# Performance work log

Hardware: AMD Instinct MI355X
Metric: run time of the kernel (lower is better)

The kernel has to match this reference:

```python
import jax, jax.numpy as jnp
import numpy as np

HEADS = 16
KV_HEADS = 8
DIMS = 64
IN_DIMS = 1024
B, S = 2, 2048


def rope(x):
    # RoPE applied over the FULL flattened last dim (heads*dims), as in the source.
    seq_len, dim = x.shape[-2], x.shape[-1]
    thetas = 1.0 / 10000 ** (jnp.arange(0, dim, 2) / dim)          # [dim/2]
    ang = jnp.arange(1, seq_len + 1)[:, None] * thetas[None, :]    # [S, dim/2] (positions start at 1)
    cos, sin = jnp.cos(ang), jnp.sin(ang)
    xe, xo = x[..., ::2], x[..., 1::2]
    real = xe * cos - xo * sin
    imag = xe * sin + xo * cos
    return jnp.stack([real, imag], axis=-1).reshape(x.shape)


def setup_inputs() -> dict:
    key = jax.random.key(0)
    k1, k2, k3, k4, k5 = jax.random.split(key, 5)
    q = jax.random.normal(k1, (B, S, IN_DIMS), dtype=jnp.float32)
    sd = 1.0 / np.sqrt(IN_DIMS)
    Wq = jax.random.normal(k2, (IN_DIMS, HEADS * DIMS), dtype=jnp.float32) * sd
    Wk = jax.random.normal(k3, (IN_DIMS, KV_HEADS * DIMS), dtype=jnp.float32) * sd
    Wv = jax.random.normal(k4, (IN_DIMS, KV_HEADS * DIMS), dtype=jnp.float32) * sd
    Wo = jax.random.normal(k5, (HEADS * DIMS, IN_DIMS), dtype=jnp.float32) / np.sqrt(HEADS * DIMS)
    return {"q": q, "Wq": Wq, "Wk": Wk, "Wv": Wv, "Wo": Wo}


def reference(q, Wq, Wk, Wv, Wo):
    batch, seq_len, in_dims = q.shape
    kv = q  # self-attention (kv=None path)
    xq = rope(q @ Wq)            # [B, S, H*D], RoPE over flattened dim
    xk = rope(kv @ Wk)           # [B, S, Hk*D]
    xv = kv @ Wv                 # [B, S, Hk*D]
    # element-wise repeat(2) on last axis, exactly as source (interleaved duplication)
    xk = jnp.repeat(xk, 2, axis=-1)   # [B, S, H*D]
    xv = jnp.repeat(xv, 2, axis=-1)
    xq = xq.reshape(batch, seq_len, HEADS, DIMS).transpose(0, 2, 1, 3)  # [B,H,S,D]
    xk = xk.reshape(batch, seq_len, HEADS, DIMS).transpose(0, 2, 3, 1)  # [B,H,D,S]
    xv = xv.reshape(batch, seq_len, HEADS, DIMS).transpose(0, 2, 1, 3)  # [B,H,S,D]
    scale = (DIMS / HEADS) ** (-0.5)  # source uses dims/heads, not 1/sqrt(dims)
    scores = jax.nn.softmax((xq @ xk) * scale, axis=-1)  # [B,H,S,S]
    out = (scores @ xv).transpose(0, 2, 1, 3).reshape(batch, seq_len, -1)
    return out @ Wo
```

## Files before the change

### kernel.cpp

```cpp
#include <hip/hip_runtime.h>
#include <hip/hip_bf16.h>
#include <math.h>

#define HEADS 16
#define KV_HEADS 8
#define DIMS 64
#define IN_DIMS 1024
#define BATCH 2
#define SEQ 2048

typedef __attribute__((ext_vector_type(8))) short short8;
typedef __attribute__((ext_vector_type(4))) float f32x4;
typedef __attribute__((ext_vector_type(4))) unsigned int u32x4;
typedef __attribute__((ext_vector_type(2))) unsigned int u32x2;

__device__ __forceinline__ short f2bf(float f) {
    __hip_bfloat16 h = __float2bfloat16(f);
    return *reinterpret_cast<short*>(&h);
}

__device__ __forceinline__ unsigned int cvtpk(float a, float b) {
    unsigned int r;
    asm("v_cvt_pk_bf16_f32 %0, %1, %2" : "=v"(r) : "v"(a), "v"(b));
    return r;
}

__device__ __forceinline__ void gl_lds16(const void* g, void* l) {
    __builtin_amdgcn_global_load_lds(
        (const __attribute__((address_space(1))) unsigned int*)g,
        (__attribute__((address_space(3))) unsigned int*)l, 16, 0, 0);
}

#define LOG2_10000 13.287712379549449f
#define CSCALE (0.5f * 1.4426950408889634f)

__global__ __launch_bounds__(256) void prep_weights(
    const float* __restrict__ Wq, const float* __restrict__ Wk,
    const float* __restrict__ Wv, const float* __restrict__ Wo,
    short* __restrict__ WT, short* __restrict__ WoPt,
    const float* __restrict__ qin, short* __restrict__ Abf)
{
    __shared__ float t[32][33];
    int z = blockIdx.z;
    if (z >= 4) {
        int i = (z - 4) * 1024 + blockIdx.y * 32 + blockIdx.x;
        size_t idx = ((size_t)i * 256 + threadIdx.x) * 8;
        float4 a = *(const float4*)(qin + idx);
        float4 c = *(const float4*)(qin + idx + 4);
        u32x4 s = { cvtpk(a.x, a.y), cvtpk(a.z, a.w),
                    cvtpk(c.x, c.y), cvtpk(c.z, c.w) };
        *(u32x4*)(Abf + idx) = s;
        return;
    }
    int bx = blockIdx.x * 32, by = blockIdx.y * 32;
    int x = threadIdx.x & 31, y = threadIdx.x >> 5;
    if (z == 3) {
        if (by >= 512) return;
        #pragma unroll
        for (int i = 0; i < 32; i += 8) {
            int d = by + y + i;
            t[y + i][x] = Wo[(size_t)(2 * d) * 1024 + bx + x]
                        + Wo[(size_t)(2 * d + 1) * 1024 + bx + x];
        }
        __syncthreads();
        #pragma unroll
        for (int i = 0; i < 32; i += 8)
            WoPt[(size_t)(bx + y + i) * 512 + by + x] = f2bf(t[x][y + i]);
    } else {
        const float* W = (z == 0) ? Wq : ((z == 1) ? Wk : Wv);
        int N = (z == 0) ? 1024 : 512;
        if (bx >= N) return;
        short* dst = WT + ((z == 0) ? 0 : ((z == 1) ? (size_t)1024 * 1024
                                                    : (size_t)1536 * 1024));
        #pragma unroll
        for (int i = 0; i < 32; i += 8)
            t[y + i][x] = W[(size_t)(by + y + i) * N + bx + x];
        __syncthreads();
        #pragma unroll
        for (int i = 0; i < 32; i += 8)
            dst[(size_t)(bx + y + i) * 1024 + by + x] = f2bf(t[x][y + i]);
    }
}

__global__ __launch_bounds__(256) void gemm_af32(
    const short* __restrict__ A, const short* __restrict__ Bt,
    float* __restrict__ C, int M, int N, int K)
{
    __shared__ short As[128][64];
    __shared__ short Bs[128][64];

    int tid  = threadIdx.x;
    int lane = tid & 63, wave = tid >> 6;
    int quad = lane >> 4, ln = lane & 15;
    int wm = (wave >> 1) * 64, wn = (wave & 1) * 64;
    int row0 = blockIdx.y * 128, col0 = blockIdx.x * 128;

    int sr = lane >> 3;
    int sk = (lane & 7) * 8;

    f32x4 acc[4][4] = {};

    for (int kt = 0; kt < K; kt += 64) {
        #pragma unroll
        for (int u = 0; u < 4; ++u) {
            int r = wave * 32 + u * 8;
            gl_lds16(A + (size_t)(row0 + r + sr) * K + kt + sk, &As[r][0]);
        }
        #pragma unroll
        for (int u = 0; u < 4; ++u) {
            int r = wave * 32 + u * 8;
            gl_lds16(Bt + (size_t)(col0 + r + sr) * K + kt + sk, &Bs[r][0]);
        }
        __syncthreads();

        #pragma unroll
        for (int k0 = 0; k0 < 64; k0 += 32) {
            short8 af[4], bfr[4];
            #pragma unroll
            for (int i = 0; i < 4; ++i)
                af[i] = *(const short8*)&As[wm + 16 * i + ln][k0 + quad * 8];
            #pragma unroll
            for (int j = 0; j < 4; ++j)
                bfr[j] = *(const short8*)&Bs[wn + 16 * j + ln][k0 + quad * 8];
            #pragma unroll
            for (int i = 0; i < 4; ++i)
                #pragma unroll
                for (int j = 0; j < 4; ++j)
                    acc[i][j] = __builtin_amdgcn_mfma_f32_16x16x32_bf16(
                        af[i], bfr[j], acc[i][j], 0, 0, 0);
        }
        __syncthreads();
    }

    #pragma unroll
    for (int i = 0; i < 4; ++i)
        #pragma unroll
        for (int j = 0; j < 4; ++j)
            #pragma unroll
            for (int r = 0; r < 4; ++r)
                C[(size_t)(row0 + wm + 16 * i + quad * 4 + r) * N
                  + col0 + wn + 16 * j + ln] = acc[i][j][r];
}

__global__ __launch_bounds__(256) void prep_qkv(
    const float* __restrict__ XQKV, short* __restrict__ Qp,
    short* __restrict__ Kb, short* __restrict__ Vtg)
{
    __shared__ float t[32][33];
    int blk = blockIdx.x;
    if (blk < 8192) {
        int idx = blk * 256 + threadIdx.x;
        int row = idx >> 9;
        int i   = idx & 511;
        int pos = row & (SEQ - 1);
        float theta = exp2f(-2.f * (float)i / 1024.f * LOG2_10000);
        float ang = (float)(pos + 1) * theta;
        float sn, cs;
        sincosf(ang, &sn, &cs);
        float2 x = *(const float2*)(XQKV + (size_t)row * 2048 + 2 * i);
        Qp[(size_t)row * 512 + i] = f2bf((x.x * (cs + sn) + x.y * (cs - sn)) * CSCALE);
    } else if (blk < 12288) {
        int idx = (blk - 8192) * 256 + threadIdx.x;
        int row = idx >> 8;
        int i   = idx & 255;
        int pos = row & (SEQ - 1);
        float theta = exp2f(-2.f * (float)i / 512.f * LOG2_10000);
        float ang = (float)(pos + 1) * theta;
        float sn, cs;
        sincosf(ang, &sn, &cs);
        float2 x = *(const float2*)(XQKV + (size_t)row * 2048 + 1024 + 2 * i);
        unsigned int o = cvtpk(x.x * cs - x.y * sn, x.x * sn + x.y * cs);
        *(unsigned int*)(Kb + (size_t)row * 512 + 2 * i) = o;
    } else {
        int id = blk - 12288;
        int bx = (id & 15) * 32;
        int by = ((id >> 4) & 63) * 32;
        int b  = id >> 10;
        int x = threadIdx.x & 31, y = threadIdx.x >> 5;
        #pragma unroll
        for (int i = 0; i < 32; i += 8)
            t[y + i][x] = XQKV[(size_t)(b * SEQ + by + y + i) * 2048 + 1536 + bx + x];
        __syncthreads();
        #pragma unroll
        for (int i = 0; i < 32; i += 8)
            Vtg[((size_t)b * 512 + bx + y + i) * SEQ + by + x] = f2bf(t[x][y + i]);
    }
}

__global__ __launch_bounds__(256) void flash_attn(
    const short* __restrict__ Qp, const short* __restrict__ Kb,
    const short* __restrict__ Vtg, short* __restrict__ AO32)
{
    __shared__ short Qs[64][40];
    __shared__ short Ks[2][64][40];
    __shared__ short Vt[2][32][72];

    int tid = threadIdx.x;
    int qt = blockIdx.x & 31;
    int h  = (blockIdx.x >> 5) & 15;
    int b  = blockIdx.x >> 9;

    int lane = tid & 63, wave = tid >> 6;
    int quad = lane >> 4, ln = lane & 15;
    int qw = wave * 16;

    {
        int row = tid >> 2, off = (tid & 3) * 8;
        *(short8*)&Qs[row][off] =
            *(const short8*)(Qp + (size_t)(b * SEQ + qt * 64 + row) * 512 + h * 32 + off);
    }

    const short* Kgb = Kb + (size_t)(b * SEQ) * 512 + 32 * h;
    const short* Vgb = Vtg + ((size_t)b * 512 + 32 * h) * SEQ;

    int krow = tid >> 2, koff = (tid & 3) * 8;
    int prow = ((krow >> 5) << 5) | (((krow >> 2) & 1) << 4)
             | (((krow >> 3) & 3) << 2) | (krow & 3);
    int vrow = tid >> 3, voff = (tid & 7) * 8;

    short8 kreg = *(const short8*)(Kgb + (size_t)krow * 512 + koff);
    short8 vreg = *(const short8*)(Vgb + (size_t)vrow * SEQ + voff);
    *(short8*)&Ks[0][prow][koff] = kreg;
    *(short8*)&Vt[0][vrow][voff] = vreg;
    __syncthreads();

    short8 af = *(const short8*)&Qs[qw + ln][quad * 8];

    float lsum = 0.f;
    f32x4 Oacc[2] = {};
    const f32x4 zz = {};

    for (int t = 0; t < 32; ++t) {
        int cur = t & 1;

        if (t < 31) {
            int ktn = (t + 1) * 64;
            kreg = *(const short8*)(Kgb + (size_t)(ktn + krow) * 512 + koff);
            vreg = *(const short8*)(Vgb + (size_t)vrow * SEQ + ktn + voff);
        }

        f32x4 sc[4];
        __builtin_amdgcn_s_setprio(1);
        #pragma unroll
        for (int j0 = 0; j0 < 4; ++j0) {
            short8 kf = *(const short8*)&Ks[cur][j0 * 16 + ln][quad * 8];
            sc[j0] = __builtin_amdgcn_mfma_f32_16x16x32_bf16(kf, af, zz, 0, 0, 0);
        }
        __builtin_amdgcn_s_setprio(0);

        short8 pf[2];
        #pragma unroll
        for (int kg = 0; kg < 2; ++kg) {
            float p0 = exp2f(sc[2 * kg][0]);
            float p1 = exp2f(sc[2 * kg][1]);
            float p2 = exp2f(sc[2 * kg][2]);
            float p3 = exp2f(sc[2 * kg][3]);
            float p4 = exp2f(sc[2 * kg + 1][0]);
            float p5 = exp2f(sc[2 * kg + 1][1]);
            float p6 = exp2f(sc[2 * kg + 1][2]);
            float p7 = exp2f(sc[2 * kg + 1][3]);
            lsum += ((p0 + p1) + (p2 + p3)) + ((p4 + p5) + (p6 + p7));
            u32x4 w = { cvtpk(p0, p1), cvtpk(p2, p3),
                        cvtpk(p4, p5), cvtpk(p6, p7) };
            pf[kg] = __builtin_bit_cast(short8, w);
        }

        __builtin_amdgcn_s_setprio(1);
        #pragma unroll
        for (int kg = 0; kg < 2; ++kg) {
            #pragma unroll
            for (int ng = 0; ng < 2; ++ng) {
                short8 vf = *(const short8*)&Vt[cur][ng * 16 + ln][kg * 32 + quad * 8];
                Oacc[ng] = __builtin_amdgcn_mfma_f32_16x16x32_bf16(
                    vf, pf[kg], Oacc[ng], 0, 0, 0);
            }
        }
        __builtin_amdgcn_s_setprio(0);

        if (t < 31) {
            *(short8*)&Ks[cur ^ 1][prow][koff] = kreg;
            *(short8*)&Vt[cur ^ 1][vrow][voff] = vreg;
        }
        __syncthreads();
    }

    lsum += __shfl_xor(lsum, 16);
    lsum += __shfl_xor(lsum, 32);
    float inv = 1.f / lsum;

    size_t row = (size_t)(b * SEQ) + qt * 64 + qw + ln;
    #pragma unroll
    for (int ng = 0; ng < 2; ++ng) {
        u32x2 o2 = { cvtpk(Oacc[ng][0] * inv, Oacc[ng][1] * inv),
                     cvtpk(Oacc[ng][2] * inv, Oacc[ng][3] * inv) };
        *(u32x2*)&AO32[row * 512 + h * 32 + ng * 16 + quad * 4] = o2;
    }
}

__global__ __launch_bounds__(256) void gemm_wo(
    const short* __restrict__ A, const short* __restrict__ Bt,
    float* __restrict__ C)
{
    __shared__ short As[64][64];
    __shared__ short Bs[128][64];

    int tid  = threadIdx.x;
    int lane = tid & 63, wave = tid >> 6;
    int quad = lane >> 4, ln = lane & 15;
    int wm = (wave >> 1) * 32, wn = (wave & 1) * 64;
    int row0 = blockIdx.y * 64, col0 = blockIdx.x * 128;
    const int K = 512, N = 1024;

    int sr = lane >> 3;
    int sk = (lane & 7) * 8;

    f32x4 acc[2][4] = {};

    for (int kt = 0; kt < K; kt += 64) {
        #pragma unroll
        for (int u = 0; u < 2; ++u) {
            int r = wave * 16 + u * 8;
            gl_lds16(A + (size_t)(row0 + r + sr) * K + kt + sk, &As[r][0]);
        }
        #pragma unroll
        for (int u = 0; u < 4; ++u) {
            int r = wave * 32 + u * 8;
            gl_lds16(Bt + (size_t)(col0 + r + sr) * K + kt + sk, &Bs[r][0]);
        }
        __syncthreads();

        #pragma unroll
        for (int k0 = 0; k0 < 64; k0 += 32) {
            short8 af[2], bfr[4];
            #pragma unroll
            for (int i = 0; i < 2; ++i)
                af[i] = *(const short8*)&As[wm + 16 * i + ln][k0 + quad * 8];
            #pragma unroll
            for (int j = 0; j < 4; ++j)
                bfr[j] = *(const short8*)&Bs[wn + 16 * j + ln][k0 + quad * 8];
            #pragma unroll
            for (int i = 0; i < 2; ++i)
                #pragma unroll
                for (int j = 0; j < 4; ++j)
                    acc[i][j] = __builtin_amdgcn_mfma_f32_16x16x32_bf16(
                        af[i], bfr[j], acc[i][j], 0, 0, 0);
        }
        __syncthreads();
    }

    #pragma unroll
    for (int i = 0; i < 2; ++i)
        #pragma unroll
        for (int j = 0; j < 4; ++j)
            #pragma unroll
            for (int r = 0; r < 4; ++r)
                C[(size_t)(row0 + wm + 16 * i + quad * 4 + r) * N
                  + col0 + wn + 16 * j + ln] = acc[i][j][r];
}

extern "C" void kernel_launch(void* const* d_in, const int* in_sizes, int n_in,
                              void* d_out, int out_size, void* d_ws, size_t ws_size,
                              hipStream_t stream)
{
    const float* q  = (const float*)d_in[0];
    const float* Wq = (const float*)d_in[1];
    const float* Wk = (const float*)d_in[2];
    const float* Wv = (const float*)d_in[3];
    const float* Wo = (const float*)d_in[4];
    float* out = (float*)d_out;

    const int M = BATCH * SEQ;

    float* XQKV = (float*)d_ws;
    short* WT   = (short*)(XQKV + (size_t)M * 2048);
    short* WoPt = WT + (size_t)2048 * 1024;
    short* Qp   = WoPt + (size_t)1024 * 512;
    short* Kb   = Qp + (size_t)M * 512;
    short* Vtg  = Kb + (size_t)M * 512;
    short* AO32 = WT;
    short* Abf  = Qp;

    dim3 blk(256);

    prep_weights<<<dim3(32, 32, 6), blk, 0, stream>>>(Wq, Wk, Wv, Wo, WT, WoPt, q, Abf);

    gemm_af32<<<dim3(16, 32), blk, 0, stream>>>(Abf, WT, XQKV, M, 2048, 1024);

    prep_qkv<<<14336, blk, 0, stream>>>(XQKV, Qp, Kb, Vtg);

    flash_attn<<<BATCH * HEADS * (SEQ / 64), blk, 0, stream>>>(Qp, Kb, Vtg, AO32);

    gemm_wo<<<dim3(8, 64), blk, 0, stream>>>(AO32, WoPt, out);
}
```

Measured before the change: 177.1 us.

## Double flash-attention query tile to 128 rows with split K/V loader threads

The flash attention kernel now uses 512-thread blocks that each cover 128 query rows, so every K/V tile staged into shared memory is reused by eight waves instead of four, and the grid shrinks by half. Threads are split so the first 256 load K and the rest load V, which halves per-thread global-load registers. The packed bf16 conversion via inline v_cvt_pk_bf16_f32 is replaced with per-element __float2bfloat16 calls, which may cost extra VALU instructions. The trade-off is fewer, larger blocks (512 blocks) and a heavier barrier per iteration, which may reduce occupancy and latency hiding.

```diff
diff --git a/kernel.cpp b/kernel.cpp
--- a/kernel.cpp
+++ b/kernel.cpp
@@ -12,7 +12,6 @@
 typedef __attribute__((ext_vector_type(8))) short short8;
 typedef __attribute__((ext_vector_type(4))) float f32x4;
 typedef __attribute__((ext_vector_type(4))) unsigned int u32x4;
-typedef __attribute__((ext_vector_type(2))) unsigned int u32x2;
 
 __device__ __forceinline__ short f2bf(float f) {
     __hip_bfloat16 h = __float2bfloat16(f);
@@ -187,18 +186,18 @@
     }
 }
 
-__global__ __launch_bounds__(256) void flash_attn(
+__global__ __launch_bounds__(512) void flash_attn(
     const short* __restrict__ Qp, const short* __restrict__ Kb,
     const short* __restrict__ Vtg, short* __restrict__ AO32)
 {
-    __shared__ short Qs[64][40];
+    __shared__ short Qs[128][40];
     __shared__ short Ks[2][64][40];
     __shared__ short Vt[2][32][72];
 
     int tid = threadIdx.x;
-    int qt = blockIdx.x & 31;
-    int h  = (blockIdx.x >> 5) & 15;
-    int b  = blockIdx.x >> 9;
+    int qt = blockIdx.x & 15;
+    int h  = (blockIdx.x >> 4) & 15;
+    int b  = blockIdx.x >> 8;
 
     int lane = tid & 63, wave = tid >> 6;
     int quad = lane >> 4, ln = lane & 15;
@@ -207,21 +206,27 @@
     {
         int row = tid >> 2, off = (tid & 3) * 8;
         *(short8*)&Qs[row][off] =
-            *(const short8*)(Qp + (size_t)(b * SEQ + qt * 64 + row) * 512 + h * 32 + off);
+            *(const short8*)(Qp + (size_t)(b * SEQ + qt * 128 + row) * 512 + h * 32 + off);
     }
 
     const short* Kgb = Kb + (size_t)(b * SEQ) * 512 + 32 * h;
     const short* Vgb = Vtg + ((size_t)b * 512 + 32 * h) * SEQ;
 
-    int krow = tid >> 2, koff = (tid & 3) * 8;
+    bool doK = tid < 256;
+    int st = tid & 255;
+    int krow = st >> 2, koff = (st & 3) * 8;
     int prow = ((krow >> 5) << 5) | (((krow >> 2) & 1) << 4)
              | (((krow >> 3) & 3) << 2) | (krow & 3);
-    int vrow = tid >> 3, voff = (tid & 7) * 8;
-
-    short8 kreg = *(const short8*)(Kgb + (size_t)krow * 512 + koff);
-    short8 vreg = *(const short8*)(Vgb + (size_t)vrow * SEQ + voff);
-    *(short8*)&Ks[0][prow][koff] = kreg;
-    *(short8*)&Vt[0][vrow][voff] = vreg;
+    int vrow = st >> 3, voff = (st & 7) * 8;
+
+    short8 sreg;
+    if (doK) {
+        sreg = *(const short8*)(Kgb + (size_t)krow * 512 + koff);
+        *(short8*)&Ks[0][prow][koff] = sreg;
+    } else {
+        sreg = *(const short8*)(Vgb + (size_t)vrow * SEQ + voff);
+        *(short8*)&Vt[0][vrow][voff] = sreg;
+    }
     __syncthreads();
 
     short8 af = *(const short8*)&Qs[qw + ln][quad * 8];
@@ -235,8 +240,10 @@
 
         if (t < 31) {
             int ktn = (t + 1) * 64;
-            kreg = *(const short8*)(Kgb + (size_t)(ktn + krow) * 512 + koff);
-            vreg = *(const short8*)(Vgb + (size_t)vrow * SEQ + ktn + voff);
+            if (doK)
+                sreg = *(const short8*)(Kgb + (size_t)(ktn + krow) * 512 + koff);
+            else
+                sreg = *(const short8*)(Vgb + (size_t)vrow * SEQ + ktn + voff);
         }
 
         f32x4 sc[4];
@@ -260,9 +267,9 @@
             float p6 = exp2f(sc[2 * kg + 1][2]);
             float p7 = exp2f(sc[2 * kg + 1][3]);
             lsum += ((p0 + p1) + (p2 + p3)) + ((p4 + p5) + (p6 + p7));
-            u32x4 w = { cvtpk(p0, p1), cvtpk(p2, p3),
-                        cvtpk(p4, p5), cvtpk(p6, p7) };
-            pf[kg] = __builtin_bit_cast(short8, w);
+            short8 s = { f2bf(p0), f2bf(p1), f2bf(p2), f2bf(p3),
+                         f2bf(p4), f2bf(p5), f2bf(p6), f2bf(p7) };
+            pf[kg] = s;
         }
 
         __builtin_amdgcn_s_setprio(1);
@@ -278,8 +285,8 @@
         __builtin_amdgcn_s_setprio(0);
 
         if (t < 31) {
-            *(short8*)&Ks[cur ^ 1][prow][koff] = kreg;
-            *(short8*)&Vt[cur ^ 1][vrow][voff] = vreg;
+            if (doK) *(short8*)&Ks[cur ^ 1][prow][koff] = sreg;
+            else     *(short8*)&Vt[cur ^ 1][vrow][voff] = sreg;
         }
         __syncthreads();
     }
@@ -288,12 +295,12 @@
     lsum += __shfl_xor(lsum, 32);
     float inv = 1.f / lsum;
 
-    size_t row = (size_t)(b * SEQ) + qt * 64 + qw + ln;
+    size_t row = (size_t)(b * SEQ) + qt * 128 + qw + ln;
     #pragma unroll
     for (int ng = 0; ng < 2; ++ng) {
-        u32x2 o2 = { cvtpk(Oacc[ng][0] * inv, Oacc[ng][1] * inv),
-                     cvtpk(Oacc[ng][2] * inv, Oacc[ng][3] * inv) };
-        *(u32x2*)&AO32[row * 512 + h * 32 + ng * 16 + quad * 4] = o2;
+        short4 o4 = { f2bf(Oacc[ng][0] * inv), f2bf(Oacc[ng][1] * inv),
+                      f2bf(Oacc[ng][2] * inv), f2bf(Oacc[ng][3] * inv) };
+        *(short4*)&AO32[row * 512 + h * 32 + ng * 16 + quad * 4] = o4;
     }
 }
 
@@ -388,7 +395,7 @@
 
     prep_qkv<<<14336, blk, 0, stream>>>(XQKV, Qp, Kb, Vtg);
 
-    flash_attn<<<BATCH * HEADS * (SEQ / 64), blk, 0, stream>>>(Qp, Kb, Vtg, AO32);
+    flash_attn<<<BATCH * HEADS * (SEQ / 128), dim3(512), 0, stream>>>(Qp, Kb, Vtg, AO32);
 
     gemm_wo<<<dim3(8, 64), blk, 0, stream>>>(AO32, WoPt, out);
 }
```

Result: faster. 173.6 us (-2.0%).
